# Performance work log

Hardware: AMD Instinct MI355X
Metric: run time of the kernel (lower is better)

The kernel has to match this reference:

```python
import jax, jax.numpy as jnp
import numpy as np

N = 8192      # number of mentions
NC = 30       # SETTINGS.n_cands
D = 300       # SETTINGS.d
WIN = 100     # context window size
TOPK = 25     # min(SETTINGS.attention_token_count, window_size)
NEG = -1e10   # mask fill value from original code


def setup_inputs() -> dict:
    key = jax.random.key(0)
    k1, k2, k3 = jax.random.split(key, 3)
    embeddings = jax.random.normal(k1, (N, NC, D), dtype=jnp.float32)
    tokenEmbeddings = jax.random.normal(k2, (N, WIN, D), dtype=jnp.float32)
    # ragged-style mask: first `len` tokens valid per mention
    lengths = jax.random.randint(k3, (N,), 1, WIN + 1)
    tokenMaskss = jnp.arange(WIN)[None, :] < lengths[:, None]
    B_diag1 = jnp.ones((D,), dtype=jnp.float32)
    B_diag2 = jnp.ones((D,), dtype=jnp.float32)
    return {
        "embeddings": embeddings,
        "tokenEmbeddings": tokenEmbeddings,
        "tokenMaskss": tokenMaskss,
        "B_diag1": B_diag1,
        "B_diag2": B_diag2,
    }


def reference(embeddings, tokenEmbeddings, tokenMaskss, B_diag1, B_diag2):
    # --- f_c: context embedding ---
    # diag_embed + matmul in torch == elementwise scale of token feature dim
    scores = jnp.einsum('ncd,nwd->ncw', embeddings, tokenEmbeddings * B_diag2)
    scores = jnp.where(tokenMaskss[:, None, :], scores, NEG)
    token_scores = jnp.max(scores, axis=1)
    best_scores, best_idx = jax.lax.top_k(token_scores, TOPK)   # (n, TOPK)
    best_tokens = jnp.take_along_axis(
        tokenEmbeddings, best_idx[:, :, None], axis=1)          # (n, TOPK, d)
    token_probs = jax.nn.softmax(best_scores, axis=1)
    # original renormalizes again (no-op numerically, kept for faithfulness)
    token_probs = token_probs / jnp.sum(token_probs, axis=1, keepdims=True)
    fcs = jnp.einsum('ntd,nt->nd', best_tokens, token_probs)    # (n, d)
    # --- psiss: diag-scaled dot with each candidate ---
    vals = jnp.einsum('ncd,nd->nc', embeddings, fcs * B_diag1)  # (n, n_cands)
    return vals
```

## Files before the change

kernel.cpp:

```cpp
#include <hip/hip_runtime.h>
#include <math.h>

#define NC    30
#define D     300
#define WIN   100
#define TOPK  25
#define NEGV  -1e10f
#define NKS   19
#define AST   312

typedef __attribute__((ext_vector_type(8)))  short short8;
typedef __attribute__((ext_vector_type(16))) float f32x16;
typedef __attribute__((ext_vector_type(4)))  unsigned int uint4v;

__device__ inline unsigned short bftrunc(float f) {
    return (unsigned short)(__builtin_bit_cast(unsigned int, f) >> 16);
}
__device__ inline float bfval(unsigned short b) {
    return __builtin_bit_cast(float, (unsigned int)b << 16);
}
__device__ inline void split8(const float* v, short8& hi, short8& lo) {
    #pragma unroll
    for (int j = 0; j < 8; ++j) {
        unsigned short hb = bftrunc(v[j]);
        float lf = v[j] - bfval(hb);
        hi[j] = (short)hb;
        lo[j] = (short)bftrunc(lf);
    }
}

__global__ __launch_bounds__(256, 4)
void fused_mention_kernel(const float* __restrict__ E,
                          const float* __restrict__ T,
                          const void*  __restrict__ maskp,
                          const float* __restrict__ B1,
                          const float* __restrict__ B2,
                          float* __restrict__ out)
{
    const int n     = blockIdx.x;
    const int tid   = threadIdx.x;
    const int wv    = tid >> 6;
    const int lane  = tid & 63;
    const int arow  = lane & 31;
    const int khalf = (lane >> 5) * 8;

    __shared__ __align__(16) short Ah[NC * AST];
    __shared__ __align__(16) short Al[NC * AST];
    __shared__ __align__(16) float fcsL[D];
    __shared__ float ts[WIN];
    __shared__ float bscore[TOPK];
    __shared__ int   bidx[TOPK];
    __shared__ float bprob[TOPK];
    __shared__ float vred[4][32];

    if (tid < WIN) ts[tid] = NEGV;

    int found;
    {
        const uint4v* m4 = (const uint4v*)maskp;
        uint4v w = m4[wv * 64 + lane];
        found = (((w.x | w.y | w.z | w.w) & 0xFFFFFF00u) != 0u) ? 1 : 0;
    }
    const bool bytemask = (__ballot(found) != 0ULL);

    int v0m = 0, v1m = 0;
    if (bytemask) {
        const unsigned char* mb = (const unsigned char*)maskp + (size_t)n * WIN;
        v0m = mb[lane] != 0;
        if (lane + 64 < WIN) v1m = mb[lane + 64] != 0;
    } else {
        const int* mi = (const int*)maskp + (size_t)n * WIN;
        v0m = mi[lane] != 0;
        if (lane + 64 < WIN) v1m = mi[lane + 64] != 0;
    }
    const int L = __popcll(__ballot(v0m)) + __popcll(__ballot(v1m));

    {
        const int srow = tid & 31;
        const int scol = tid >> 5;
        if (srow < NC) {
            #pragma unroll
            for (int k = 0; k < 5; ++k) {
                const int c8 = scol + 8 * k;
                if (c8 < 38) {
                    const int col = c8 * 8;
                    const float* src = E + ((size_t)n * NC + srow) * D + col;
                    float v[8];
                    float4 q0 = *reinterpret_cast<const float4*>(src);
                    float4 b0 = *reinterpret_cast<const float4*>(B2 + col);
                    v[0] = q0.x * b0.x; v[1] = q0.y * b0.y;
                    v[2] = q0.z * b0.z; v[3] = q0.w * b0.w;
                    if (c8 < 37) {
                        float4 q1 = *reinterpret_cast<const float4*>(src + 4);
                        float4 b1 = *reinterpret_cast<const float4*>(B2 + col + 4);
                        v[4] = q1.x * b1.x; v[5] = q1.y * b1.y;
                        v[6] = q1.z * b1.z; v[7] = q1.w * b1.w;
                    } else {
                        v[4] = v[5] = v[6] = v[7] = 0.f;
                    }
                    short8 hi, lo;
                    split8(v, hi, lo);
                    *reinterpret_cast<short8*>(Ah + srow * AST + col) = hi;
                    *reinterpret_cast<short8*>(Al + srow * AST + col) = lo;
                }
            }
        }
    }
    __syncthreads();
    const int ntiles = (L + 31) >> 5;
    const float* Tn = T + (size_t)n * WIN * D;

    if (wv < ntiles) {
        const int t0 = wv * 32;
        const float* bp = Tn + (size_t)min(t0 + arow, L - 1) * D;
        const int aoff = min(arow, NC - 1) * AST + khalf;
        f32x16 c;
        #pragma unroll
        for (int r = 0; r < 16; ++r) c[r] = 0.f;

        float4 q0r[4], q1r[4];
        #pragma unroll
        for (int s = 0; s < 4; ++s) {
            const int kb = 16 * s + khalf;
            q0r[s] = *reinterpret_cast<const float4*>(bp + kb);
            q1r[s] = *reinterpret_cast<const float4*>(bp + kb + 4);
        }
        #pragma unroll
        for (int s = 0; s < NKS; ++s) {
            const int slot = s & 3;
            float4 q0 = q0r[slot], q1 = q1r[slot];
            if (s + 4 < NKS) {
                const int kb2 = 16 * (s + 4) + khalf;
                q0r[slot] = *reinterpret_cast<const float4*>(bp + kb2);
                q1r[slot] = (kb2 + 8 <= D)
                          ? *reinterpret_cast<const float4*>(bp + kb2 + 4)
                          : make_float4(0.f, 0.f, 0.f, 0.f);
            }
            short8 ah = *reinterpret_cast<const short8*>(Ah + aoff + 16 * s);
            short8 al = *reinterpret_cast<const short8*>(Al + aoff + 16 * s);
            float v[8] = {q0.x, q0.y, q0.z, q0.w, q1.x, q1.y, q1.z, q1.w};
            short8 bh, bl;
            split8(v, bh, bl);
            c = __builtin_amdgcn_mfma_f32_32x32x16_bf16(ah, bh, c, 0, 0, 0);
            c = __builtin_amdgcn_mfma_f32_32x32x16_bf16(al, bh, c, 0, 0, 0);
            c = __builtin_amdgcn_mfma_f32_32x32x16_bf16(ah, bl, c, 0, 0, 0);
        }
        if (lane >= 32) { c[14] = -__builtin_inff(); c[15] = -__builtin_inff(); }
        float m = c[0];
        #pragma unroll
        for (int r = 1; r < 16; ++r) m = fmaxf(m, c[r]);
        m = fmaxf(m, __shfl_xor(m, 32));
        if (lane < 32 && t0 + arow < L) ts[t0 + arow] = m;
    }
    __syncthreads();

    if (tid < 64) {
        float va = ts[tid];
        float vb = (tid + 64 < WIN) ? ts[tid + 64] : -__builtin_inff();
        float mx = 0.f;
        for (int t = 0; t < TOPK; ++t) {
            float v0; int i0;
            if (vb > va) { v0 = vb; i0 = tid + 64; } else { v0 = va; i0 = tid; }
            #pragma unroll
            for (int s = 32; s >= 1; s >>= 1) {
                float ov = __shfl_xor(v0, s);
                int   oi = __shfl_xor(i0, s);
                if (ov > v0 || (ov == v0 && oi < i0)) { v0 = ov; i0 = oi; }
            }
            if (t == 0) mx = v0;
            if (tid == 0) { bscore[t] = v0; bidx[t] = i0; }
            if (i0 == tid) va = -__builtin_inff();
            else if (i0 == tid + 64) vb = -__builtin_inff();
        }
        float sc = (tid < TOPK) ? bscore[tid] : 0.f;
        float p  = (tid < TOPK) ? expf(sc - mx) : 0.f;
        float s1 = p;
        #pragma unroll
        for (int s = 32; s >= 1; s >>= 1) s1 += __shfl_xor(s1, s);
        p = p / s1;
        float s2 = p;
        #pragma unroll
        for (int s = 32; s >= 1; s >>= 1) s2 += __shfl_xor(s2, s);
        p = p / s2;
        if (tid < TOPK) bprob[tid] = p;
    }
    __syncthreads();

    for (int d = tid; d < D; d += 256) {
        float acc = 0.f;
        #pragma unroll 5
        for (int t = 0; t < TOPK; ++t)
            acc += bprob[t] * Tn[(size_t)bidx[t] * D + d];
        fcsL[d] = acc;
    }
    __syncthreads();

    {
        const int dg = tid >> 5;
        const int d0 = dg * 40;
        const bool full = (dg < 7);
        const int cg = arow;
        const bool cok = (cg < NC);
        float acc2 = 0.f;
        const float* Erow = E + ((size_t)n * NC + (cok ? cg : 0)) * D + d0;
        #pragma unroll
        for (int j = 0; j < 5; ++j) {
            float4 ev = *reinterpret_cast<const float4*>(Erow + 4 * j);
            float4 bv = *reinterpret_cast<const float4*>(B1 + d0 + 4 * j);
            float4 fv = *reinterpret_cast<const float4*>(fcsL + d0 + 4 * j);
            acc2 += ev.x * bv.x * fv.x + ev.y * bv.y * fv.y
                  + ev.z * bv.z * fv.z + ev.w * bv.w * fv.w;
        }
        if (full) {
            #pragma unroll
            for (int j = 5; j < 10; ++j) {
                float4 ev = *reinterpret_cast<const float4*>(Erow + 4 * j);
                float4 bv = *reinterpret_cast<const float4*>(B1 + d0 + 4 * j);
                float4 fv = *reinterpret_cast<const float4*>(fcsL + d0 + 4 * j);
                acc2 += ev.x * bv.x * fv.x + ev.y * bv.y * fv.y
                      + ev.z * bv.z * fv.z + ev.w * bv.w * fv.w;
            }
        }
        if (!cok) acc2 = 0.f;
        acc2 += __shfl_xor(acc2, 32);
        if (lane < 32) vred[wv][cg] = acc2;
    }
    __syncthreads();
    if (tid < NC) {
        out[(size_t)n * NC + tid] =
            vred[0][tid] + vred[1][tid] + vred[2][tid] + vred[3][tid];
    }
}

extern "C" void kernel_launch(void* const* d_in, const int* in_sizes, int n_in,
                              void* d_out, int out_size, void* d_ws, size_t ws_size,
                              hipStream_t stream)
{
    const float* E  = (const float*)d_in[0];
    const float* T  = (const float*)d_in[1];
    const void*  M  = d_in[2];
    const float* B1 = (const float*)d_in[3];
    const float* B2 = (const float*)d_in[4];
    float* out = (float*)d_out;
    const int n = in_sizes[0] / (NC * D);
    fused_mention_kernel<<<n, 256, 0, stream>>>(E, T, M, B1, B2, out);
}
```

Before: 318.3 us.

## Reuse MFMA score tiles for output when B1 equals B2, skipping token regather

When B1 and B2 are elementwise equal (checked at runtime), the output equals a probability-weighted sum of the already computed candidate-token score columns. The kernel accumulates the selected columns from the MFMA accumulators with warp shuffles instead of regathering the top-k token rows from global memory and redoing the dot products. It also issues the first token prefetch loads before the barrier that follows the staging of the candidate matrix into shared memory. The fast path relies on a data-dependent equality check and reuses split-bf16 scores, which can differ slightly numerically from the fp32 path.

```diff
diff --git a/kernel.cpp b/kernel.cpp
--- a/kernel.cpp
+++ b/kernel.cpp
@@ -51,7 +51,7 @@
     __shared__ float bscore[TOPK];
     __shared__ int   bidx[TOPK];
     __shared__ float bprob[TOPK];
-    __shared__ float vred[4][32];
+    __shared__ float vredS[4][32];
 
     if (tid < WIN) ts[tid] = NEGV;
 
@@ -73,7 +73,16 @@
         v0m = mi[lane] != 0;
         if (lane + 64 < WIN) v1m = mi[lane + 64] != 0;
     }
-    const int L = __popcll(__ballot(v0m)) + __popcll(__ballot(v1m));
+    const int L  = __popcll(__ballot(v0m)) + __popcll(__ballot(v1m));
+    const int Lc = (L > 0) ? L : 1;
+
+    int neq = 0;
+    #pragma unroll
+    for (int k = 0; k < 5; ++k) {
+        const int d = lane + 64 * k;
+        if (d < D) neq |= (B1[d] != B2[d]) ? 1 : 0;
+    }
+    const bool beq = (__ballot(neq) == 0ULL);
 
     {
         const int srow = tid & 31;
@@ -106,25 +115,28 @@
             }
         }
     }
-    __syncthreads();
+
     const int ntiles = (L + 31) >> 5;
     const float* Tn = T + (size_t)n * WIN * D;
-
+    const float* bp = Tn + (size_t)min(wv * 32 + arow, Lc - 1) * D;
+
+    float4 q0r[4], q1r[4];
     if (wv < ntiles) {
-        const int t0 = wv * 32;
-        const float* bp = Tn + (size_t)min(t0 + arow, L - 1) * D;
-        const int aoff = min(arow, NC - 1) * AST + khalf;
-        f32x16 c;
-        #pragma unroll
-        for (int r = 0; r < 16; ++r) c[r] = 0.f;
-
-        float4 q0r[4], q1r[4];
         #pragma unroll
         for (int s = 0; s < 4; ++s) {
             const int kb = 16 * s + khalf;
             q0r[s] = *reinterpret_cast<const float4*>(bp + kb);
             q1r[s] = *reinterpret_cast<const float4*>(bp + kb + 4);
         }
+    }
+    __syncthreads();
+
+    f32x16 c;
+    #pragma unroll
+    for (int r = 0; r < 16; ++r) c[r] = 0.f;
+    if (wv < ntiles) {
+        const int t0 = wv * 32;
+        const int aoff = min(arow, NC - 1) * AST + khalf;
         #pragma unroll
         for (int s = 0; s < NKS; ++s) {
             const int slot = s & 3;
@@ -186,49 +198,86 @@
     }
     __syncthreads();
 
-    for (int d = tid; d < D; d += 256) {
-        float acc = 0.f;
-        #pragma unroll 5
-        for (int t = 0; t < TOPK; ++t)
-            acc += bprob[t] * Tn[(size_t)bidx[t] * D + d];
-        fcsL[d] = acc;
-    }
-    __syncthreads();
-
-    {
-        const int dg = tid >> 5;
-        const int d0 = dg * 40;
-        const bool full = (dg < 7);
-        const int cg = arow;
-        const bool cok = (cg < NC);
-        float acc2 = 0.f;
-        const float* Erow = E + ((size_t)n * NC + (cok ? cg : 0)) * D + d0;
-        #pragma unroll
-        for (int j = 0; j < 5; ++j) {
-            float4 ev = *reinterpret_cast<const float4*>(Erow + 4 * j);
-            float4 bv = *reinterpret_cast<const float4*>(B1 + d0 + 4 * j);
-            float4 fv = *reinterpret_cast<const float4*>(fcsL + d0 + 4 * j);
-            acc2 += ev.x * bv.x * fv.x + ev.y * bv.y * fv.y
-                  + ev.z * bv.z * fv.z + ev.w * bv.w * fv.w;
-        }
-        if (full) {
-            #pragma unroll
-            for (int j = 5; j < 10; ++j) {
+    if (beq) {
+        float vacc[16];
+        #pragma unroll
+        for (int r = 0; r < 16; ++r) vacc[r] = 0.f;
+        if (wv < ntiles) {
+            for (int t = 0; t < TOPK; ++t) {
+                const int ix = bidx[t];
+                if ((ix >> 5) == wv) {
+                    const float p = bprob[t];
+                    if ((lane & 31) == (ix & 31)) {
+                        #pragma unroll
+                        for (int r = 0; r < 16; ++r) vacc[r] += p * c[r];
+                    }
+                }
+            }
+        }
+        #pragma unroll
+        for (int r = 0; r < 16; ++r) {
+            float s = vacc[r];
+            s += __shfl_xor(s, 1);  s += __shfl_xor(s, 2);
+            s += __shfl_xor(s, 4);  s += __shfl_xor(s, 8);
+            s += __shfl_xor(s, 16);
+            vacc[r] = s;
+        }
+        if ((lane & 31) == 0) {
+            #pragma unroll
+            for (int r = 0; r < 16; ++r) {
+                const int row = (r & 3) + 8 * (r >> 2) + 4 * (lane >> 5);
+                vredS[wv][row] = vacc[r];
+            }
+        }
+        __syncthreads();
+        if (tid < NC) {
+            out[(size_t)n * NC + tid] = vredS[0][tid] + vredS[1][tid]
+                                      + vredS[2][tid] + vredS[3][tid];
+        }
+    } else {
+        for (int d = tid; d < D; d += 256) {
+            float acc = 0.f;
+            #pragma unroll 5
+            for (int t = 0; t < TOPK; ++t)
+                acc += bprob[t] * Tn[(size_t)bidx[t] * D + d];
+            fcsL[d] = acc;
+        }
+        __syncthreads();
+        {
+            const int dg = tid >> 5;
+            const int d0 = dg * 40;
+            const bool full = (dg < 7);
+            const int cg = arow;
+            const bool cok = (cg < NC);
+            float acc2 = 0.f;
+            const float* Erow = E + ((size_t)n * NC + (cok ? cg : 0)) * D + d0;
+            #pragma unroll
+            for (int j = 0; j < 5; ++j) {
                 float4 ev = *reinterpret_cast<const float4*>(Erow + 4 * j);
                 float4 bv = *reinterpret_cast<const float4*>(B1 + d0 + 4 * j);
                 float4 fv = *reinterpret_cast<const float4*>(fcsL + d0 + 4 * j);
                 acc2 += ev.x * bv.x * fv.x + ev.y * bv.y * fv.y
                       + ev.z * bv.z * fv.z + ev.w * bv.w * fv.w;
             }
-        }
-        if (!cok) acc2 = 0.f;
-        acc2 += __shfl_xor(acc2, 32);
-        if (lane < 32) vred[wv][cg] = acc2;
-    }
-    __syncthreads();
-    if (tid < NC) {
-        out[(size_t)n * NC + tid] =
-            vred[0][tid] + vred[1][tid] + vred[2][tid] + vred[3][tid];
+            if (full) {
+                #pragma unroll
+                for (int j = 5; j < 10; ++j) {
+                    float4 ev = *reinterpret_cast<const float4*>(Erow + 4 * j);
+                    float4 bv = *reinterpret_cast<const float4*>(B1 + d0 + 4 * j);
+                    float4 fv = *reinterpret_cast<const float4*>(fcsL + d0 + 4 * j);
+                    acc2 += ev.x * bv.x * fv.x + ev.y * bv.y * fv.y
+                          + ev.z * bv.z * fv.z + ev.w * bv.w * fv.w;
+                }
+            }
+            if (!cok) acc2 = 0.f;
+            acc2 += __shfl_xor(acc2, 32);
+            if (lane < 32) vredS[wv][cg] = acc2;
+        }
+        __syncthreads();
+        if (tid < NC) {
+            out[(size_t)n * NC + tid] = vredS[0][tid] + vredS[1][tid]
+                                      + vredS[2][tid] + vredS[3][tid];
+        }
     }
 }
 
```

Result: faster. 278.1 us (-12.6%).
